# Performance work log

Hardware: AMD Instinct MI355X
Metric: run time of the kernel (lower is better)

Reference implementation:

```python
import jax, jax.numpy as jnp
import numpy as np

N_NODES = 10000
N_EDGES = 640000
IN_CH, HID, OUT_CH = 128, 128, 64


def _gcn_conv(x, edge_index, edge_weight, W, b, n_nodes):
    # PyG GCNConv (default add_self_loops=True, normalize=True, bias=True):
    #   A_hat = A + I ; D = rowsum(A_hat) ; norm_e = D^-1/2[src] * w_e * D^-1/2[dst]
    #   out[dst] += norm_e * (x @ W)[src] ; out += b
    src, dst = edge_index[0], edge_index[1]
    loop = jnp.arange(n_nodes, dtype=edge_index.dtype)
    src = jnp.concatenate([src, loop])
    dst = jnp.concatenate([dst, loop])
    w = jnp.concatenate([edge_weight, jnp.ones((n_nodes,), edge_weight.dtype)])
    deg = jax.ops.segment_sum(w, dst, num_segments=n_nodes)  # scatter on col
    dinv = jnp.where(deg > 0, jax.lax.rsqrt(deg), 0.0).astype(x.dtype)
    norm = dinv[src] * w * dinv[dst]  # [E+N]
    xw = x @ W  # dense GEMM [N, out]
    msg = norm[:, None] * xw[src]  # gather + scale [E+N, out]
    out = jax.ops.segment_sum(msg, dst, num_segments=n_nodes)  # scatter-add
    return out + b


def setup_inputs() -> dict:
    key = jax.random.key(0)
    ks = jax.random.split(key, 8)
    x = jax.random.normal(ks[0], (N_NODES, IN_CH), dtype=jnp.float32)
    edge_index = jax.random.randint(ks[1], (2, N_EDGES), 0, N_NODES, dtype=jnp.int64)
    edge_weight = jax.random.uniform(ks[2], (N_EDGES,), dtype=jnp.float32)
    W1 = jax.random.normal(ks[3], (IN_CH, HID), dtype=jnp.float32) * 0.05
    b1 = jnp.zeros((HID,), jnp.float32)
    W2 = jax.random.normal(ks[4], (HID, OUT_CH), dtype=jnp.float32) * 0.05
    b2 = jnp.zeros((OUT_CH,), jnp.float32)
    return {"x": x, "edge_index": edge_index, "edge_weight": edge_weight,
            "W1": W1, "b1": b1, "W2": W2, "b2": b2}


def reference(x, edge_index, edge_weight, W1, b1, W2, b2):
    h = _gcn_conv(x, edge_index, edge_weight, W1, b1, N_NODES)
    h = jax.nn.relu(h)
    out = _gcn_conv(h, edge_index, edge_weight, W2, b2, N_NODES)
    return out
```

## Files before the change

### kernel.cpp

```cpp
#include <hip/hip_runtime.h>
#include <math.h>

#define N_NODES 10000
#define N_EDGES 640000
#define K_DIM   128
#define OUT_CH  64
#define ELLW    192

#define CHUNKS  128
#define CHUNK_E 5000
#define GB      313

typedef unsigned long long ull;
typedef unsigned int uint;
typedef unsigned short ushort;
typedef unsigned char uchar;

#define FIXED_SCALE 262144.0f


__device__ __forceinline__ float bf2f(ushort u) {
    return __uint_as_float(((uint)u) << 16);
}
__device__ __forceinline__ ushort f2bf(float v) {
    uint u = __float_as_uint(v);
    uint r = u + 0x7fffu + ((u >> 16) & 1u);
    return (ushort)(r >> 16);
}

template <int NCOL>
__device__ void gemm_body(const float* __restrict__ A, const float* __restrict__ B,
                          ushort* __restrict__ C, int blk, int M,
                          float* sA , float* sB ) {
    constexpr int K = 128;
    constexpr int TM = 32;
    constexpr int KT = 32;
    constexpr int R = 256 / NCOL;
    constexpr int RPT = TM / R;
    int tid = threadIdx.x;
    int c = tid % NCOL;
    int rr = tid / NCOL;
    int row0 = blk * TM;
    float acc[RPT];
#pragma unroll
    for (int r = 0; r < RPT; ++r) acc[r] = 0.0f;

    for (int k0 = 0; k0 < K; k0 += KT) {
        for (int i = tid; i < TM * KT; i += 256) {
            int r = i / KT, k = i % KT;
            int gr = row0 + r;
            sA[r * (KT + 1) + k] = (gr < M) ? A[gr * K + k0 + k] : 0.0f;
        }
        for (int i = tid; i < KT * NCOL; i += 256) {
            int k = i / NCOL, cc = i % NCOL;
            sB[k * NCOL + cc] = B[(k0 + k) * NCOL + cc];
        }
        __syncthreads();
#pragma unroll
        for (int k = 0; k < KT; ++k) {
            float b = sB[k * NCOL + c];
#pragma unroll
            for (int r = 0; r < RPT; ++r)
                acc[r] += sA[(rr * RPT + r) * (KT + 1) + k] * b;
        }
        __syncthreads();
    }
#pragma unroll
    for (int r = 0; r < RPT; ++r) {
        int gr = row0 + rr * RPT + r;
        if (gr < M) C[gr * NCOL + c] = f2bf(acc[r]);
    }
}

__global__ __launch_bounds__(256) void preA_gemm1_kernel(const int* __restrict__ ei,
                                                         const float* __restrict__ ew,
                                                         uchar* __restrict__ rank8,
                                                         uint* __restrict__ sd32,
                                                         uint* __restrict__ blockcnt,
                                                         const float* __restrict__ x,
                                                         const float* __restrict__ W1,
                                                         ushort* __restrict__ xw1b) {
    __shared__ uint smem[N_NODES];
    if (blockIdx.x < CHUNKS) {
        const int c = blockIdx.x;
        const int tid = threadIdx.x;
        __shared__ int sflag;
        if (tid == 0) sflag = 0;
        for (int i = tid; i < N_NODES; i += 256) smem[i] = 0u;
        __syncthreads();
        int a = (tid < 64) ? ei[2 * (c * CHUNK_E + tid) + 1] : 0;
        if (a) atomicOr(&sflag, 1);
        __syncthreads();
        const int f = sflag;
        const ull* ei64 = (const ull*)ei;
        for (int k = tid; k < CHUNK_E; k += 256) {
            int e = c * CHUNK_E + k;
            int s, d;
            if (f) { s = ei[e];        d = ei[N_EDGES + e]; }
            else   { s = (int)ei64[e]; d = (int)ei64[N_EDGES + e]; }
            float w = ew[e];
            uint fx = (uint)(w * FIXED_SCALE + 0.5f);
            uint old = atomicAdd(&smem[d], (1u << 24) | fx);
            rank8[e] = (uchar)(old >> 24);
            sd32[e] = ((uint)d << 16) | (uint)s;
        }
        __syncthreads();
        for (int i = tid; i < N_NODES; i += 256)
            blockcnt[c * N_NODES + i] = smem[i];
    } else {
        float* sA = (float*)smem;
        float* sB = sA + 32 * 33;
        gemm_body<128>(x, W1, xw1b, blockIdx.x - CHUNKS, N_NODES, sA, sB);
    }
}

__global__ __launch_bounds__(256) void scanB_kernel(const uint* __restrict__ blockcnt,
                                                    uchar* __restrict__ base8,
                                                    int* __restrict__ cnt_arr,
                                                    float* __restrict__ dinv) {
    int n = blockIdx.x * 256 + threadIdx.x;
    if (n >= N_NODES) return;
    uint wsum = 0;
    int run = 0;
#pragma unroll 8
    for (int c = 0; c < CHUNKS; ++c) {
        uint v = blockcnt[c * N_NODES + n];
        base8[c * N_NODES + n] = (uchar)run;
        run += (int)(v >> 24);
        wsum += v & 0xffffffu;
    }
    cnt_arr[n] = run;
    float dg = 1.0f + (float)wsum * (1.0f / FIXED_SCALE);
    dinv[n] = (float)(1.0 / sqrt((double)dg));
}

#define FILL_SPLIT 4
#define FILL_PART  (CHUNK_E / FILL_SPLIT)
__global__ __launch_bounds__(256) void fillC_kernel(const uint* __restrict__ sd32,
                                                    const float* __restrict__ ew,
                                                    const uchar* __restrict__ rank8,
                                                    const uchar* __restrict__ base8,
                                                    const float* __restrict__ dinv,
                                                    ull* __restrict__ epack) {
    const int c = blockIdx.x / FILL_SPLIT;
    const int p = blockIdx.x % FILL_SPLIT;
    const int k0 = p * FILL_PART;
    for (int k = k0 + threadIdx.x; k < k0 + FILL_PART; k += 256) {
        int e = c * CHUNK_E + k;
        uint sd = sd32[e];
        int s = (int)(sd & 0xffffu);
        int d = (int)(sd >> 16);
        float nrm = dinv[s] * ew[e] * dinv[d];
        int slot = (int)base8[c * N_NODES + d] + (int)rank8[e];
        if (slot < ELLW)
            epack[d * ELLW + slot] = ((ull)__float_as_uint(nrm) << 32) | (ull)(uint)s;
    }
}

__global__ __launch_bounds__(256) void gemm2_kernel(const float* __restrict__ A,
                                                    const float* __restrict__ B,
                                                    ushort* __restrict__ C) {
    __shared__ float sA[32 * 33];
    __shared__ float sB[32 * 64];
    gemm_body<64>(A, B, C, blockIdx.x, N_NODES, sA, sB);
}

template <int C, bool RELU>
__global__ __launch_bounds__(C) void aggregate_kernel(const ushort* __restrict__ xwb,
                                                      const ull* __restrict__ epack,
                                                      const int* __restrict__ cnt_arr,
                                                      const float* __restrict__ dinv,
                                                      const float* __restrict__ bias,
                                                      float* __restrict__ out) {
    __shared__ int s_src[C];
    __shared__ float s_p[C];
    int node = blockIdx.x;
    int c = threadIdx.x;
    int cnt = cnt_arr[node];
    if (cnt > ELLW) cnt = ELLW;
    float dn = dinv[node];
    float acc = dn * dn * bf2f(xwb[node * C + c]);
    int base = node * ELLW;
    for (int b = 0; b < cnt; b += C) {
        int m = cnt - b;
        if (m > C) m = C;
        if (c < m) {
            ull v = epack[base + b + c];
            s_src[c] = (int)(uint)(v & 0xffffffffULL);
            s_p[c] = __uint_as_float((uint)(v >> 32));
        }
        __syncthreads();
#pragma unroll 4
        for (int j = 0; j < m; ++j)
            acc += s_p[j] * bf2f(xwb[s_src[j] * C + c]);
        __syncthreads();
    }
    acc += bias[c];
    if (RELU) acc = fmaxf(acc, 0.0f);
    out[node * C + c] = acc;
}

extern "C" void kernel_launch(void* const* d_in, const int* in_sizes, int n_in,
                              void* d_out, int out_size, void* d_ws, size_t ws_size,
                              hipStream_t stream) {
    const float* x  = (const float*)d_in[0];
    const int*   ei = (const int*)d_in[1];
    const float* ew = (const float*)d_in[2];
    const float* W1 = (const float*)d_in[3];
    const float* b1 = (const float*)d_in[4];
    const float* W2 = (const float*)d_in[5];
    const float* b2 = (const float*)d_in[6];
    float* out = (float*)d_out;

    char* ws = (char*)d_ws;
    ushort* xw1b    = (ushort*)(ws + 0);
    float*  h       = (float*) (ws + 2560000);
    ushort* xw2b    = (ushort*)(ws + 7680000);
    ull*    epack   = (ull*)   (ws + 8960000);
    uint*   blockcnt= (uint*)  (ws + 24320000);
    uchar*  base8   = (uchar*) (ws + 29440000);
    uchar*  rank8   = (uchar*) (ws + 30720000);
    uint*   sd32    = (uint*)  (ws + 31360000);
    int*    cnt_arr = (int*)   (ws + 33920000);
    float*  dinv    = (float*) (ws + 33960000);

    preA_gemm1_kernel<<<CHUNKS + GB, 256, 0, stream>>>(ei, ew, rank8, sd32, blockcnt, x, W1, xw1b);
    scanB_kernel<<<(N_NODES + 255) / 256, 256, 0, stream>>>(blockcnt, base8, cnt_arr, dinv);
    fillC_kernel<<<CHUNKS * FILL_SPLIT, 256, 0, stream>>>(sd32, ew, rank8, base8, dinv, epack);
    aggregate_kernel<128, true><<<N_NODES, 128, 0, stream>>>(xw1b, epack, cnt_arr, dinv, b1, h);
    gemm2_kernel<<<GB, 256, 0, stream>>>(h, W2, xw2b);
    aggregate_kernel<64, false><<<N_NODES, 64, 0, stream>>>(xw2b, epack, cnt_arr, dinv, b2, out);
}
```

Before: 169.5 us.

## Aggregate one node per wavefront with shuffled edge lists and packed bf16 loads

Replaces the block-per-node aggregation kernels with kernels that handle one node per 64-lane wavefront, four nodes per 256-thread block. Edge indices and norms are broadcast with wave shuffles instead of shared memory plus __syncthreads. Each lane loads two bf16 channels as one 32-bit word. The 64-channel layer splits the wave into two halves that process alternate edges and combine their partial sums with a shuffle. This removes barrier overhead and tiny 64-thread blocks and widens the gather loads, at the cost of more shuffle instructions and unused lanes on the final odd edge.

Result: slower. 187.6 us (+10.6%).

```diff
diff --git a/kernel.cpp b/kernel.cpp
--- a/kernel.cpp
+++ b/kernel.cpp
@@ -21,6 +21,12 @@
 
 __device__ __forceinline__ float bf2f(ushort u) {
     return __uint_as_float(((uint)u) << 16);
+}
+__device__ __forceinline__ float bf_lo(uint u) {
+    return __uint_as_float(u << 16);
+}
+__device__ __forceinline__ float bf_hi(uint u) {
+    return __uint_as_float(u & 0xffff0000u);
 }
 __device__ __forceinline__ ushort f2bf(float v) {
     uint u = __float_as_uint(v);
@@ -165,39 +171,93 @@
     gemm_body<64>(A, B, C, blockIdx.x, N_NODES, sA, sB);
 }
 
-template <int C, bool RELU>
-__global__ __launch_bounds__(C) void aggregate_kernel(const ushort* __restrict__ xwb,
-                                                      const ull* __restrict__ epack,
-                                                      const int* __restrict__ cnt_arr,
-                                                      const float* __restrict__ dinv,
-                                                      const float* __restrict__ bias,
-                                                      float* __restrict__ out) {
-    __shared__ int s_src[C];
-    __shared__ float s_p[C];
-    int node = blockIdx.x;
-    int c = threadIdx.x;
+__global__ __launch_bounds__(256) void agg1_kernel(const ushort* __restrict__ xwb,
+                                                   const ull* __restrict__ epack,
+                                                   const int* __restrict__ cnt_arr,
+                                                   const float* __restrict__ dinv,
+                                                   const float* __restrict__ bias,
+                                                   float* __restrict__ out) {
+    const uint* __restrict__ xw32 = (const uint*)xwb;
+    int w = threadIdx.x >> 6;
+    int l = threadIdx.x & 63;
+    int node = blockIdx.x * 4 + w;
     int cnt = cnt_arr[node];
     if (cnt > ELLW) cnt = ELLW;
     float dn = dinv[node];
-    float acc = dn * dn * bf2f(xwb[node * C + c]);
-    int base = node * ELLW;
-    for (int b = 0; b < cnt; b += C) {
+    uint su = xw32[node * 64 + l];
+    float acc0 = dn * dn * bf_lo(su);
+    float acc1 = dn * dn * bf_hi(su);
+    const ull* ep = epack + (long)node * ELLW;
+    for (int b = 0; b < cnt; b += 64) {
         int m = cnt - b;
-        if (m > C) m = C;
-        if (c < m) {
-            ull v = epack[base + b + c];
-            s_src[c] = (int)(uint)(v & 0xffffffffULL);
-            s_p[c] = __uint_as_float((uint)(v >> 32));
-        }
-        __syncthreads();
+        if (m > 64) m = 64;
+        ull v = (l < m) ? ep[b + l] : 0ULL;
+        int sl = (int)(uint)(v & 0xffffffffULL);
+        float nl = __uint_as_float((uint)(v >> 32));
 #pragma unroll 4
-        for (int j = 0; j < m; ++j)
-            acc += s_p[j] * bf2f(xwb[s_src[j] * C + c]);
-        __syncthreads();
-    }
-    acc += bias[c];
-    if (RELU) acc = fmaxf(acc, 0.0f);
-    out[node * C + c] = acc;
+        for (int j = 0; j < m; ++j) {
+            int s = __shfl(sl, j);
+            float n = __shfl(nl, j);
+            uint u = xw32[s * 64 + l];
+            acc0 = fmaf(n, bf_lo(u), acc0);
+            acc1 = fmaf(n, bf_hi(u), acc1);
+        }
+    }
+    float2 bb = ((const float2*)bias)[l];
+    float2 o;
+    o.x = fmaxf(acc0 + bb.x, 0.0f);
+    o.y = fmaxf(acc1 + bb.y, 0.0f);
+    ((float2*)out)[node * 64 + l] = o;
+}
+
+__global__ __launch_bounds__(256) void agg2_kernel(const ushort* __restrict__ xwb,
+                                                   const ull* __restrict__ epack,
+                                                   const int* __restrict__ cnt_arr,
+                                                   const float* __restrict__ dinv,
+                                                   const float* __restrict__ bias,
+                                                   float* __restrict__ out) {
+    const uint* __restrict__ xw32 = (const uint*)xwb;
+    int w = threadIdx.x >> 6;
+    int lane = threadIdx.x & 63;
+    int p = lane >> 5;
+    int q = lane & 31;
+    int node = blockIdx.x * 4 + w;
+    int cnt = cnt_arr[node];
+    if (cnt > ELLW) cnt = ELLW;
+    float dn = dinv[node];
+    float acc0 = 0.0f, acc1 = 0.0f;
+    if (p == 0) {
+        uint su = xw32[node * 32 + q];
+        acc0 = dn * dn * bf_lo(su);
+        acc1 = dn * dn * bf_hi(su);
+    }
+    const ull* ep = epack + (long)node * ELLW;
+    for (int b = 0; b < cnt; b += 64) {
+        int m = cnt - b;
+        if (m > 64) m = 64;
+        ull v = (lane < m) ? ep[b + lane] : 0ULL;
+        int sl = (int)(uint)(v & 0xffffffffULL);
+        float nl = __uint_as_float((uint)(v >> 32));
+        int iters = (m + 1) >> 1;
+#pragma unroll 4
+        for (int i = 0; i < iters; ++i) {
+            int j = 2 * i + p;
+            int s = __shfl(sl, j);
+            float n = __shfl(nl, j);
+            uint u = xw32[s * 32 + q];
+            acc0 = fmaf(n, bf_lo(u), acc0);
+            acc1 = fmaf(n, bf_hi(u), acc1);
+        }
+    }
+    acc0 += __shfl_xor(acc0, 32);
+    acc1 += __shfl_xor(acc1, 32);
+    if (p == 0) {
+        float2 bb = ((const float2*)bias)[q];
+        float2 o;
+        o.x = acc0 + bb.x;
+        o.y = acc1 + bb.y;
+        ((float2*)out)[node * 32 + q] = o;
+    }
 }
 
 extern "C" void kernel_launch(void* const* d_in, const int* in_sizes, int n_in,
@@ -227,7 +287,7 @@
     preA_gemm1_kernel<<<CHUNKS + GB, 256, 0, stream>>>(ei, ew, rank8, sd32, blockcnt, x, W1, xw1b);
     scanB_kernel<<<(N_NODES + 255) / 256, 256, 0, stream>>>(blockcnt, base8, cnt_arr, dinv);
     fillC_kernel<<<CHUNKS * FILL_SPLIT, 256, 0, stream>>>(sd32, ew, rank8, base8, dinv, epack);
-    aggregate_kernel<128, true><<<N_NODES, 128, 0, stream>>>(xw1b, epack, cnt_arr, dinv, b1, h);
+    agg1_kernel<<<N_NODES / 4, 256, 0, stream>>>(xw1b, epack, cnt_arr, dinv, b1, h);
     gemm2_kernel<<<GB, 256, 0, stream>>>(h, W2, xw2b);
-    aggregate_kernel<64, false><<<N_NODES, 64, 0, stream>>>(xw2b, epack, cnt_arr, dinv, b2, out);
-}
+    agg2_kernel<<<N_NODES / 4, 256, 0, stream>>>(xw2b, epack, cnt_arr, dinv, b2, out);
+}
```
